# Performance work log

Measured on AMD Instinct MI355X. Metric: run time of the kernel, lower is better.

The kernel has to match this reference:

```python
import jax, jax.numpy as jnp
import numpy as np

N_NODES = 1_000_000
N_EDGES = 16_000_000
NUM_GRAPHS = 64
LATENT = 128
LAMBDA_LAP = 0.1
LAMBDA_DRIFT = 0.01
LAMBDA_ARAP = 0.1
BETA_WARMUP = 10
BETA_FINAL = 1.0


def setup_inputs() -> dict:
    key = jax.random.key(0)
    k1, k2, k3, k4, k5, k6 = jax.random.split(key, 6)
    return {
        "pred_output": jax.random.normal(k1, (N_NODES, 2), dtype=jnp.float32),
        "target": jax.random.normal(k2, (N_NODES, 2), dtype=jnp.float32),
        "edge_index": jax.random.randint(k3, (2, N_EDGES), 0, N_NODES, dtype=jnp.int32),
        "batch_indices": jnp.sort(jax.random.randint(k4, (N_NODES,), 0, NUM_GRAPHS, dtype=jnp.int32)),
        "mu": jax.random.normal(k5, (NUM_GRAPHS, LATENT), dtype=jnp.float32),
        "logvar": jax.random.normal(k6, (NUM_GRAPHS, LATENT), dtype=jnp.float32),
        "epoch": 5,
    }


def reference(pred_output, target, edge_index, batch_indices, mu, logvar, epoch):
    # reconstruction: MSE, mean over all elements
    recon = jnp.mean((pred_output - target) ** 2)

    # edge gather once; laplacian and ARAP reuse the same diff tensor
    i, j = edge_index[0], edge_index[1]
    diff = pred_output[i] - pred_output[j]                 # [E, 2]
    lap = jnp.sum(diff ** 2) / edge_index.shape[1]

    # drift suppression: per-graph mean displacement via segment_sum
    ones = jnp.ones((pred_output.shape[0],), dtype=pred_output.dtype)
    sums = jax.ops.segment_sum(pred_output, batch_indices, num_segments=NUM_GRAPHS)
    counts = jax.ops.segment_sum(ones, batch_indices, num_segments=NUM_GRAPHS)
    means = sums / counts[:, None]                         # [G, 2]
    drift = jnp.sum(means ** 2) / NUM_GRAPHS

    # ARAP: unbiased variance of edge lengths (torch.var default ddof=1)
    edge_len = jnp.sqrt(jnp.sum(diff ** 2, axis=1))        # [E]
    arap = jnp.var(edge_len, ddof=1)

    # KL divergence, mean over graphs
    kl = jnp.mean(-0.5 * jnp.sum(1.0 + logvar - mu ** 2 - jnp.exp(logvar), axis=1))

    # beta warmup (epoch is a static python int)
    beta = (epoch / BETA_WARMUP) * BETA_FINAL if epoch < BETA_WARMUP else BETA_FINAL

    total = recon + LAMBDA_LAP * lap + LAMBDA_DRIFT * drift + LAMBDA_ARAP * arap + beta * kl
    return total
```

## Files before the change

### kernel.cpp

```cpp
#include <hip/hip_runtime.h>
#include <hip/hip_fp16.h>
#include <math.h>

#define N_NODES    1000000
#define N_EDGES    16000000
#define NUM_GRAPHS 64
#define LATENT     128

#define WS_DOUBLES 200
#define PACKED_OFFSET 2048

typedef int vint4 __attribute__((ext_vector_type(4)));

__global__ void init_ws(double* ws) {
    int t = blockIdx.x * blockDim.x + threadIdx.x;
    if (t < WS_DOUBLES) ws[t] = 0.0;
}

__global__ void node_kl_pass(const float2* __restrict__ pred,
                             const float2* __restrict__ targ,
                             const int*    __restrict__ batch,
                             const float*  __restrict__ mu,
                             const float*  __restrict__ logvar,
                             double* __restrict__ ws,
                             unsigned* __restrict__ packed) {
    __shared__ float sgx[NUM_GRAPHS];
    __shared__ float sgy[NUM_GRAPHS];
    __shared__ int   scnt[NUM_GRAPHS];
    __shared__ double smem[8];

    for (int g = threadIdx.x; g < NUM_GRAPHS; g += blockDim.x) {
        sgx[g] = 0.f; sgy[g] = 0.f; scnt[g] = 0;
    }
    __syncthreads();

    float recon = 0.f;
    const int idx = blockIdx.x * blockDim.x + threadIdx.x;
    const int stride = gridDim.x * blockDim.x;
    for (int n = idx; n < N_NODES; n += stride) {
        float2 p = pred[n];
        float2 t = targ[n];
        float dx = p.x - t.x, dy = p.y - t.y;
        recon += dx * dx + dy * dy;

        if (packed) {
            __half2 h = __floats2half2_rn(p.x, p.y);
            packed[n] = *reinterpret_cast<unsigned*>(&h);
        }

        int b = batch[n];
        unsigned long long act = __ballot(1);
        int b0 = __shfl(b, 0);
        bool fast = (act == ~0ull) && (__ballot(b == b0) == act);
        if (fast) {
            float sx = p.x, sy = p.y;
            #pragma unroll
            for (int off = 32; off > 0; off >>= 1) {
                sx += __shfl_xor(sx, off);
                sy += __shfl_xor(sy, off);
            }
            if ((threadIdx.x & 63) == 0) {
                atomicAdd(&sgx[b0], sx);
                atomicAdd(&sgy[b0], sy);
                atomicAdd(&scnt[b0], 64);
            }
        } else {
            atomicAdd(&sgx[b], p.x);
            atomicAdd(&sgy[b], p.y);
            atomicAdd(&scnt[b], 1);
        }
    }

    double r = (double)recon;
    #pragma unroll
    for (int off = 32; off > 0; off >>= 1) r += __shfl_down(r, off);
    const int lane = threadIdx.x & 63;
    const int wid  = threadIdx.x >> 6;
    if (lane == 0) smem[wid] = r;
    __syncthreads();
    if (threadIdx.x == 0) {
        double tot = 0.0;
        const int nw = blockDim.x >> 6;
        for (int w = 0; w < nw; ++w) tot += smem[w];
        atomicAdd(&ws[0], tot);
    }

    for (int g = threadIdx.x; g < NUM_GRAPHS; g += blockDim.x) {
        if (scnt[g] != 0) {
            atomicAdd(&ws[4 + g],   (double)sgx[g]);
            atomicAdd(&ws[68 + g],  (double)sgy[g]);
            atomicAdd(&ws[132 + g], (double)scnt[g]);
        }
    }

    if (blockIdx.x == 0) {
        double s = 0.0;
        for (int t = threadIdx.x; t < NUM_GRAPHS * LATENT; t += blockDim.x) {
            float m = mu[t], lv = logvar[t];
            s += (double)(1.0f + lv - m * m - expf(lv));
        }
        #pragma unroll
        for (int off = 32; off > 0; off >>= 1) s += __shfl_down(s, off);
        __syncthreads();
        if (lane == 0) smem[wid] = s;
        __syncthreads();
        if (threadIdx.x == 0) {
            double tot = 0.0;
            const int nw = blockDim.x >> 6;
            for (int w = 0; w < nw; ++w) tot += smem[w];
            atomicAdd(&ws[3], tot);
        }
    }
}

__device__ __forceinline__ void edge_flush(float s1, float s2, double* ws,
                                           double* smem1, double* smem2) {
    double r1 = (double)s1, r2 = (double)s2;
    #pragma unroll
    for (int off = 32; off > 0; off >>= 1) {
        r1 += __shfl_down(r1, off);
        r2 += __shfl_down(r2, off);
    }
    const int lane = threadIdx.x & 63;
    const int wid  = threadIdx.x >> 6;
    if (lane == 0) { smem1[wid] = r1; smem2[wid] = r2; }
    __syncthreads();
    if (threadIdx.x == 0) {
        double t1 = 0.0, t2 = 0.0;
        const int nw = blockDim.x >> 6;
        for (int w = 0; w < nw; ++w) { t1 += smem1[w]; t2 += smem2[w]; }
        atomicAdd(&ws[1], t1);
        atomicAdd(&ws[2], t2);
    }
}

__device__ __forceinline__ vint4 ld_stream_x4(const vint4* p) {
    vint4 r;
    asm volatile("global_load_dwordx4 %0, %1, off sc0 sc1 nt"
                 : "=v"(r) : "v"(p) : "memory");
    return r;
}

__device__ __forceinline__ void acc_pair(unsigned pa, unsigned pb,
                                         float& s1, float& s2) {
    __half2 ha = *reinterpret_cast<__half2*>(&pa);
    __half2 hb = *reinterpret_cast<__half2*>(&pb);
    float2 fa = __half22float2(ha);
    float2 fb = __half22float2(hb);
    float dx = fa.x - fb.x, dy = fa.y - fb.y;
    float l2 = dx * dx + dy * dy;
    s2 += l2;
    s1 += sqrtf(l2);
}

__global__ void edge_pass_packed(const unsigned* __restrict__ packed,
                                 const int* __restrict__ ei,
                                 double* __restrict__ ws) {
    __shared__ double smem1[8];
    __shared__ double smem2[8];

    float s1 = 0.f, s2 = 0.f;
    const int gid = blockIdx.x * blockDim.x + threadIdx.x;
    const int stride = gridDim.x * blockDim.x;
    const int ngroups = N_EDGES / 8;
    const vint4* eia = (const vint4*)ei;
    const vint4* eib = (const vint4*)(ei + N_EDGES);

    int g = gid;
    if (g < ngroups) {
        vint4 a0 = ld_stream_x4(eia + 2 * g);
        vint4 a1 = ld_stream_x4(eia + 2 * g + 1);
        vint4 b0 = ld_stream_x4(eib + 2 * g);
        vint4 b1 = ld_stream_x4(eib + 2 * g + 1);
        asm volatile("s_waitcnt vmcnt(0)"
                     : "+v"(a0), "+v"(a1), "+v"(b0), "+v"(b1) :: "memory");
        __builtin_amdgcn_sched_barrier(0);
        while (true) {
            const int gn = g + stride;
            const bool more = gn < ngroups;
            vint4 a0n = {0,0,0,0}, a1n = {0,0,0,0};
            vint4 b0n = {0,0,0,0}, b1n = {0,0,0,0};
            if (more) {
                a0n = ld_stream_x4(eia + 2 * gn);
                a1n = ld_stream_x4(eia + 2 * gn + 1);
                b0n = ld_stream_x4(eib + 2 * gn);
                b1n = ld_stream_x4(eib + 2 * gn + 1);
            }

            unsigned qa0 = packed[a0.x], qb0 = packed[b0.x];
            unsigned qa1 = packed[a0.y], qb1 = packed[b0.y];
            unsigned qa2 = packed[a0.z], qb2 = packed[b0.z];
            unsigned qa3 = packed[a0.w], qb3 = packed[b0.w];
            unsigned qa4 = packed[a1.x], qb4 = packed[b1.x];
            unsigned qa5 = packed[a1.y], qb5 = packed[b1.y];
            unsigned qa6 = packed[a1.z], qb6 = packed[b1.z];
            unsigned qa7 = packed[a1.w], qb7 = packed[b1.w];

            acc_pair(qa0, qb0, s1, s2);
            acc_pair(qa1, qb1, s1, s2);
            acc_pair(qa2, qb2, s1, s2);
            acc_pair(qa3, qb3, s1, s2);
            acc_pair(qa4, qb4, s1, s2);
            acc_pair(qa5, qb5, s1, s2);
            acc_pair(qa6, qb6, s1, s2);
            acc_pair(qa7, qb7, s1, s2);

            if (!more) break;
            asm volatile("s_waitcnt vmcnt(0)"
                         : "+v"(a0n), "+v"(a1n), "+v"(b0n), "+v"(b1n) :: "memory");
            __builtin_amdgcn_sched_barrier(0);
            g = gn; a0 = a0n; a1 = a1n; b0 = b0n; b1 = b1n;
        }
    }
    asm volatile("s_waitcnt vmcnt(0)" ::: "memory");
    edge_flush(s1, s2, ws, smem1, smem2);
}

__global__ void edge_pass_f32(const float2* __restrict__ pred,
                              const int* __restrict__ ei,
                              double* __restrict__ ws) {
    __shared__ double smem1[8];
    __shared__ double smem2[8];

    float s1 = 0.f, s2 = 0.f;
    const int idx = blockIdx.x * blockDim.x + threadIdx.x;
    const int stride = gridDim.x * blockDim.x;
    for (int e = idx; e < N_EDGES; e += stride) {
        int i = ei[e];
        int j = ei[N_EDGES + e];
        float2 pi = pred[i];
        float2 pj = pred[j];
        float dx = pi.x - pj.x, dy = pi.y - pj.y;
        float l2 = dx * dx + dy * dy;
        s2 += l2;
        s1 += sqrtf(l2);
    }
    edge_flush(s1, s2, ws, smem1, smem2);
}

__global__ void finalize(const double* __restrict__ ws,
                         const int* __restrict__ epoch_p,
                         float* __restrict__ out) {
    double recon = ws[0] / (2.0 * (double)N_NODES);
    double S1 = ws[1], S2 = ws[2];
    double lap  = S2 / (double)N_EDGES;
    double arap = (S2 - S1 * S1 / (double)N_EDGES) / ((double)N_EDGES - 1.0);
    double drift = 0.0;
    for (int g = 0; g < NUM_GRAPHS; ++g) {
        double c  = ws[132 + g];
        double mx = ws[4 + g] / c;
        double my = ws[68 + g] / c;
        drift += mx * mx + my * my;
    }
    drift /= (double)NUM_GRAPHS;
    double kl = -0.5 * ws[3] / (double)NUM_GRAPHS;
    int epoch = *epoch_p;
    double beta = (epoch < 10) ? ((double)epoch / 10.0) : 1.0;
    out[0] = (float)(recon + 0.1 * lap + 0.01 * drift + 0.1 * arap + beta * kl);
}

extern "C" void kernel_launch(void* const* d_in, const int* in_sizes, int n_in,
                              void* d_out, int out_size, void* d_ws, size_t ws_size,
                              hipStream_t stream) {
    const float2* pred   = (const float2*)d_in[0];
    const float2* targ   = (const float2*)d_in[1];
    const int*    ei     = (const int*)d_in[2];
    const int*    batch  = (const int*)d_in[3];
    const float*  mu     = (const float*)d_in[4];
    const float*  logvar = (const float*)d_in[5];
    const int*    epoch  = (const int*)d_in[6];
    float* out = (float*)d_out;
    double* ws = (double*)d_ws;

    const bool use_packed = ws_size >= (size_t)PACKED_OFFSET + 4ull * N_NODES;
    unsigned* packed = use_packed
        ? (unsigned*)((char*)d_ws + PACKED_OFFSET) : (unsigned*)nullptr;

    init_ws<<<1, 256, 0, stream>>>(ws);
    node_kl_pass<<<1024, 256, 0, stream>>>(pred, targ, batch, mu, logvar, ws, packed);
    if (use_packed)
        edge_pass_packed<<<2048, 256, 0, stream>>>(packed, ei, ws);
    else
        edge_pass_f32<<<2048, 256, 0, stream>>>(pred, ei, ws);
    finalize<<<1, 1, 0, stream>>>(ws, epoch, out);
}
```

Measured before the change: 379.8 us.

## Split edge pass into four variant kernels, reorder gathers before prefetch, shard atomics

The edge pass now runs as four kernels over quarters of the edge list. Two use 8-edge groups and two use 16-edge groups, and each comes with and without the sc0 cache hint on the gathers. Inside the loop the node gathers are issued before the next index prefetch, with a partial vmcnt wait, so the gathers overlap the streaming index loads. Global double atomics are spread across shadow copies (8 for node stats, 16 for edge sums) and summed in finalize to reduce contention. The extra launches and the exploratory mix of variants add overhead and make the cause of any change unclear.

```diff
diff --git a/kernel.cpp b/kernel.cpp
--- a/kernel.cpp
+++ b/kernel.cpp
@@ -7,14 +7,21 @@
 #define NUM_GRAPHS 64
 #define LATENT     128
 
-#define WS_DOUBLES 200
-#define PACKED_OFFSET 2048
+#define SH_BASE        8
+#define SH_STRIDE      200
+#define NSHADOW_BIG    8
+#define EDGE_SH_BASE   1608
+#define EDGE_NSHADOW   16
+#define WS_DOUBLES_TOT 1736
+#define WS_DOUBLES_LEGACY 208
+#define PACKED_OFFSET_BIG    16384
+#define PACKED_OFFSET_LEGACY 2048
 
 typedef int vint4 __attribute__((ext_vector_type(4)));
 
-__global__ void init_ws(double* ws) {
+__global__ void init_ws(double* ws, int n) {
     int t = blockIdx.x * blockDim.x + threadIdx.x;
-    if (t < WS_DOUBLES) ws[t] = 0.0;
+    if (t < n) ws[t] = 0.0;
 }
 
 __global__ void node_kl_pass(const float2* __restrict__ pred,
@@ -23,7 +30,8 @@
                              const float*  __restrict__ mu,
                              const float*  __restrict__ logvar,
                              double* __restrict__ ws,
-                             unsigned* __restrict__ packed) {
+                             unsigned* __restrict__ packed,
+                             int ns) {
     __shared__ float sgx[NUM_GRAPHS];
     __shared__ float sgy[NUM_GRAPHS];
     __shared__ int   scnt[NUM_GRAPHS];
@@ -33,6 +41,8 @@
         sgx[g] = 0.f; sgy[g] = 0.f; scnt[g] = 0;
     }
     __syncthreads();
+
+    double* shbase = ws + SH_BASE + (size_t)(blockIdx.x & (ns - 1)) * SH_STRIDE;
 
     float recon = 0.f;
     const int idx = blockIdx.x * blockDim.x + threadIdx.x;
@@ -82,14 +92,14 @@
         double tot = 0.0;
         const int nw = blockDim.x >> 6;
         for (int w = 0; w < nw; ++w) tot += smem[w];
-        atomicAdd(&ws[0], tot);
+        atomicAdd(&shbase[0], tot);
     }
 
     for (int g = threadIdx.x; g < NUM_GRAPHS; g += blockDim.x) {
         if (scnt[g] != 0) {
-            atomicAdd(&ws[4 + g],   (double)sgx[g]);
-            atomicAdd(&ws[68 + g],  (double)sgy[g]);
-            atomicAdd(&ws[132 + g], (double)scnt[g]);
+            atomicAdd(&shbase[2 + g],   (double)sgx[g]);
+            atomicAdd(&shbase[66 + g],  (double)sgy[g]);
+            atomicAdd(&shbase[130 + g], (double)scnt[g]);
         }
     }
 
@@ -108,12 +118,13 @@
             double tot = 0.0;
             const int nw = blockDim.x >> 6;
             for (int w = 0; w < nw; ++w) tot += smem[w];
-            atomicAdd(&ws[3], tot);
+            atomicAdd(&shbase[1], tot);
         }
     }
 }
 
 __device__ __forceinline__ void edge_flush(float s1, float s2, double* ws,
+                                           int edge_mode,
                                            double* smem1, double* smem2) {
     double r1 = (double)s1, r2 = (double)s2;
     #pragma unroll
@@ -129,8 +140,14 @@
         double t1 = 0.0, t2 = 0.0;
         const int nw = blockDim.x >> 6;
         for (int w = 0; w < nw; ++w) { t1 += smem1[w]; t2 += smem2[w]; }
-        atomicAdd(&ws[1], t1);
-        atomicAdd(&ws[2], t2);
+        if (edge_mode) {
+            const int sh = blockIdx.x & (EDGE_NSHADOW - 1);
+            atomicAdd(&ws[EDGE_SH_BASE + sh * 8 + 0], t1);
+            atomicAdd(&ws[EDGE_SH_BASE + sh * 8 + 1], t2);
+        } else {
+            atomicAdd(&ws[1], t1);
+            atomicAdd(&ws[2], t2);
+        }
     }
 }
 
@@ -138,6 +155,18 @@
     vint4 r;
     asm volatile("global_load_dwordx4 %0, %1, off sc0 sc1 nt"
                  : "=v"(r) : "v"(p) : "memory");
+    return r;
+}
+
+template<bool SC0>
+__device__ __forceinline__ unsigned gth(const unsigned* base, int idx) {
+    unsigned r;
+    if constexpr (SC0)
+        asm volatile("global_load_dword %0, %1, %2 sc0"
+                     : "=v"(r) : "v"(idx * 4), "s"(base) : "memory");
+    else
+        asm volatile("global_load_dword %0, %1, %2"
+                     : "=v"(r) : "v"(idx * 4), "s"(base) : "memory");
     return r;
 }
 
@@ -153,72 +182,182 @@
     s1 += sqrtf(l2);
 }
 
-__global__ void edge_pass_packed(const unsigned* __restrict__ packed,
-                                 const int* __restrict__ ei,
-                                 double* __restrict__ ws) {
+template<bool SC0>
+__global__ void edge_pass8(const unsigned* __restrict__ packed,
+                           const int* __restrict__ ei,
+                           double* __restrict__ ws,
+                           int edge_mode, int g0, int ngroups) {
     __shared__ double smem1[8];
     __shared__ double smem2[8];
 
     float s1 = 0.f, s2 = 0.f;
     const int gid = blockIdx.x * blockDim.x + threadIdx.x;
     const int stride = gridDim.x * blockDim.x;
-    const int ngroups = N_EDGES / 8;
     const vint4* eia = (const vint4*)ei;
     const vint4* eib = (const vint4*)(ei + N_EDGES);
 
     int g = gid;
     if (g < ngroups) {
-        vint4 a0 = ld_stream_x4(eia + 2 * g);
-        vint4 a1 = ld_stream_x4(eia + 2 * g + 1);
-        vint4 b0 = ld_stream_x4(eib + 2 * g);
-        vint4 b1 = ld_stream_x4(eib + 2 * g + 1);
+        vint4 a0 = ld_stream_x4(eia + 2 * (g0 + g));
+        vint4 a1 = ld_stream_x4(eia + 2 * (g0 + g) + 1);
+        vint4 b0 = ld_stream_x4(eib + 2 * (g0 + g));
+        vint4 b1 = ld_stream_x4(eib + 2 * (g0 + g) + 1);
         asm volatile("s_waitcnt vmcnt(0)"
                      : "+v"(a0), "+v"(a1), "+v"(b0), "+v"(b1) :: "memory");
         __builtin_amdgcn_sched_barrier(0);
         while (true) {
+            unsigned q0  = gth<SC0>(packed, a0.x), q1  = gth<SC0>(packed, b0.x);
+            unsigned q2  = gth<SC0>(packed, a0.y), q3  = gth<SC0>(packed, b0.y);
+            unsigned q4  = gth<SC0>(packed, a0.z), q5  = gth<SC0>(packed, b0.z);
+            unsigned q6  = gth<SC0>(packed, a0.w), q7  = gth<SC0>(packed, b0.w);
+            unsigned q8  = gth<SC0>(packed, a1.x), q9  = gth<SC0>(packed, b1.x);
+            unsigned q10 = gth<SC0>(packed, a1.y), q11 = gth<SC0>(packed, b1.y);
+            unsigned q12 = gth<SC0>(packed, a1.z), q13 = gth<SC0>(packed, b1.z);
+            unsigned q14 = gth<SC0>(packed, a1.w), q15 = gth<SC0>(packed, b1.w);
+
             const int gn = g + stride;
             const bool more = gn < ngroups;
-            vint4 a0n = {0,0,0,0}, a1n = {0,0,0,0};
-            vint4 b0n = {0,0,0,0}, b1n = {0,0,0,0};
-            if (more) {
-                a0n = ld_stream_x4(eia + 2 * gn);
-                a1n = ld_stream_x4(eia + 2 * gn + 1);
-                b0n = ld_stream_x4(eib + 2 * gn);
-                b1n = ld_stream_x4(eib + 2 * gn + 1);
-            }
-
-            unsigned qa0 = packed[a0.x], qb0 = packed[b0.x];
-            unsigned qa1 = packed[a0.y], qb1 = packed[b0.y];
-            unsigned qa2 = packed[a0.z], qb2 = packed[b0.z];
-            unsigned qa3 = packed[a0.w], qb3 = packed[b0.w];
-            unsigned qa4 = packed[a1.x], qb4 = packed[b1.x];
-            unsigned qa5 = packed[a1.y], qb5 = packed[b1.y];
-            unsigned qa6 = packed[a1.z], qb6 = packed[b1.z];
-            unsigned qa7 = packed[a1.w], qb7 = packed[b1.w];
-
-            acc_pair(qa0, qb0, s1, s2);
-            acc_pair(qa1, qb1, s1, s2);
-            acc_pair(qa2, qb2, s1, s2);
-            acc_pair(qa3, qb3, s1, s2);
-            acc_pair(qa4, qb4, s1, s2);
-            acc_pair(qa5, qb5, s1, s2);
-            acc_pair(qa6, qb6, s1, s2);
-            acc_pair(qa7, qb7, s1, s2);
+            const int gs = g0 + (more ? gn : g);
+            vint4 A0 = ld_stream_x4(eia + 2 * gs);
+            vint4 A1 = ld_stream_x4(eia + 2 * gs + 1);
+            vint4 B0 = ld_stream_x4(eib + 2 * gs);
+            vint4 B1 = ld_stream_x4(eib + 2 * gs + 1);
+
+            asm volatile("s_waitcnt vmcnt(4)"
+                         : "+v"(q0), "+v"(q1), "+v"(q2), "+v"(q3),
+                           "+v"(q4), "+v"(q5), "+v"(q6), "+v"(q7),
+                           "+v"(q8), "+v"(q9), "+v"(q10), "+v"(q11),
+                           "+v"(q12), "+v"(q13), "+v"(q14), "+v"(q15)
+                         :: "memory");
+            __builtin_amdgcn_sched_barrier(0);
+
+            acc_pair(q0, q1, s1, s2);
+            acc_pair(q2, q3, s1, s2);
+            acc_pair(q4, q5, s1, s2);
+            acc_pair(q6, q7, s1, s2);
+            acc_pair(q8, q9, s1, s2);
+            acc_pair(q10, q11, s1, s2);
+            acc_pair(q12, q13, s1, s2);
+            acc_pair(q14, q15, s1, s2);
 
             if (!more) break;
             asm volatile("s_waitcnt vmcnt(0)"
-                         : "+v"(a0n), "+v"(a1n), "+v"(b0n), "+v"(b1n) :: "memory");
+                         : "+v"(A0), "+v"(A1), "+v"(B0), "+v"(B1) :: "memory");
             __builtin_amdgcn_sched_barrier(0);
-            g = gn; a0 = a0n; a1 = a1n; b0 = b0n; b1 = b1n;
+            g = gn; a0 = A0; a1 = A1; b0 = B0; b1 = B1;
         }
     }
     asm volatile("s_waitcnt vmcnt(0)" ::: "memory");
-    edge_flush(s1, s2, ws, smem1, smem2);
+    edge_flush(s1, s2, ws, edge_mode, smem1, smem2);
+}
+
+template<bool SC0>
+__global__ void edge_pass16(const unsigned* __restrict__ packed,
+                            const int* __restrict__ ei,
+                            double* __restrict__ ws,
+                            int edge_mode, int g0, int ngroups) {
+    __shared__ double smem1[8];
+    __shared__ double smem2[8];
+
+    float s1 = 0.f, s2 = 0.f;
+    const int gid = blockIdx.x * blockDim.x + threadIdx.x;
+    const int stride = gridDim.x * blockDim.x;
+    const vint4* eia = (const vint4*)ei;
+    const vint4* eib = (const vint4*)(ei + N_EDGES);
+
+    int g = gid;
+    if (g < ngroups) {
+        vint4 a0 = ld_stream_x4(eia + 4 * (g0 + g));
+        vint4 a1 = ld_stream_x4(eia + 4 * (g0 + g) + 1);
+        vint4 a2 = ld_stream_x4(eia + 4 * (g0 + g) + 2);
+        vint4 a3 = ld_stream_x4(eia + 4 * (g0 + g) + 3);
+        vint4 b0 = ld_stream_x4(eib + 4 * (g0 + g));
+        vint4 b1 = ld_stream_x4(eib + 4 * (g0 + g) + 1);
+        vint4 b2 = ld_stream_x4(eib + 4 * (g0 + g) + 2);
+        vint4 b3 = ld_stream_x4(eib + 4 * (g0 + g) + 3);
+        asm volatile("s_waitcnt vmcnt(0)"
+                     : "+v"(a0), "+v"(a1), "+v"(a2), "+v"(a3),
+                       "+v"(b0), "+v"(b1), "+v"(b2), "+v"(b3) :: "memory");
+        __builtin_amdgcn_sched_barrier(0);
+        while (true) {
+            unsigned q0  = gth<SC0>(packed, a0.x), q1  = gth<SC0>(packed, b0.x);
+            unsigned q2  = gth<SC0>(packed, a0.y), q3  = gth<SC0>(packed, b0.y);
+            unsigned q4  = gth<SC0>(packed, a0.z), q5  = gth<SC0>(packed, b0.z);
+            unsigned q6  = gth<SC0>(packed, a0.w), q7  = gth<SC0>(packed, b0.w);
+            unsigned q8  = gth<SC0>(packed, a1.x), q9  = gth<SC0>(packed, b1.x);
+            unsigned q10 = gth<SC0>(packed, a1.y), q11 = gth<SC0>(packed, b1.y);
+            unsigned q12 = gth<SC0>(packed, a1.z), q13 = gth<SC0>(packed, b1.z);
+            unsigned q14 = gth<SC0>(packed, a1.w), q15 = gth<SC0>(packed, b1.w);
+            unsigned q16 = gth<SC0>(packed, a2.x), q17 = gth<SC0>(packed, b2.x);
+            unsigned q18 = gth<SC0>(packed, a2.y), q19 = gth<SC0>(packed, b2.y);
+            unsigned q20 = gth<SC0>(packed, a2.z), q21 = gth<SC0>(packed, b2.z);
+            unsigned q22 = gth<SC0>(packed, a2.w), q23 = gth<SC0>(packed, b2.w);
+            unsigned q24 = gth<SC0>(packed, a3.x), q25 = gth<SC0>(packed, b3.x);
+            unsigned q26 = gth<SC0>(packed, a3.y), q27 = gth<SC0>(packed, b3.y);
+            unsigned q28 = gth<SC0>(packed, a3.z), q29 = gth<SC0>(packed, b3.z);
+            unsigned q30 = gth<SC0>(packed, a3.w), q31 = gth<SC0>(packed, b3.w);
+
+            const int gn = g + stride;
+            const bool more = gn < ngroups;
+            const int gs = g0 + (more ? gn : g);
+            vint4 A0 = ld_stream_x4(eia + 4 * gs);
+            vint4 A1 = ld_stream_x4(eia + 4 * gs + 1);
+            vint4 A2 = ld_stream_x4(eia + 4 * gs + 2);
+            vint4 A3 = ld_stream_x4(eia + 4 * gs + 3);
+            vint4 B0 = ld_stream_x4(eib + 4 * gs);
+            vint4 B1 = ld_stream_x4(eib + 4 * gs + 1);
+            vint4 B2 = ld_stream_x4(eib + 4 * gs + 2);
+            vint4 B3 = ld_stream_x4(eib + 4 * gs + 3);
+
+            asm volatile("s_waitcnt vmcnt(8)"
+                         : "+v"(q0), "+v"(q1), "+v"(q2), "+v"(q3),
+                           "+v"(q4), "+v"(q5), "+v"(q6), "+v"(q7),
+                           "+v"(q8), "+v"(q9), "+v"(q10), "+v"(q11),
+                           "+v"(q12), "+v"(q13), "+v"(q14), "+v"(q15)
+                         :: "memory");
+            asm volatile("s_waitcnt vmcnt(8)"
+                         : "+v"(q16), "+v"(q17), "+v"(q18), "+v"(q19),
+                           "+v"(q20), "+v"(q21), "+v"(q22), "+v"(q23),
+                           "+v"(q24), "+v"(q25), "+v"(q26), "+v"(q27),
+                           "+v"(q28), "+v"(q29), "+v"(q30), "+v"(q31)
+                         :: "memory");
+            __builtin_amdgcn_sched_barrier(0);
+
+            acc_pair(q0, q1, s1, s2);
+            acc_pair(q2, q3, s1, s2);
+            acc_pair(q4, q5, s1, s2);
+            acc_pair(q6, q7, s1, s2);
+            acc_pair(q8, q9, s1, s2);
+            acc_pair(q10, q11, s1, s2);
+            acc_pair(q12, q13, s1, s2);
+            acc_pair(q14, q15, s1, s2);
+            acc_pair(q16, q17, s1, s2);
+            acc_pair(q18, q19, s1, s2);
+            acc_pair(q20, q21, s1, s2);
+            acc_pair(q22, q23, s1, s2);
+            acc_pair(q24, q25, s1, s2);
+            acc_pair(q26, q27, s1, s2);
+            acc_pair(q28, q29, s1, s2);
+            acc_pair(q30, q31, s1, s2);
+
+            if (!more) break;
+            asm volatile("s_waitcnt vmcnt(0)"
+                         : "+v"(A0), "+v"(A1), "+v"(A2), "+v"(A3),
+                           "+v"(B0), "+v"(B1), "+v"(B2), "+v"(B3) :: "memory");
+            __builtin_amdgcn_sched_barrier(0);
+            g = gn;
+            a0 = A0; a1 = A1; a2 = A2; a3 = A3;
+            b0 = B0; b1 = B1; b2 = B2; b3 = B3;
+        }
+    }
+    asm volatile("s_waitcnt vmcnt(0)" ::: "memory");
+    edge_flush(s1, s2, ws, edge_mode, smem1, smem2);
 }
 
 __global__ void edge_pass_f32(const float2* __restrict__ pred,
                               const int* __restrict__ ei,
-                              double* __restrict__ ws) {
+                              double* __restrict__ ws,
+                              int edge_mode) {
     __shared__ double smem1[8];
     __shared__ double smem2[8];
 
@@ -235,25 +374,44 @@
         s2 += l2;
         s1 += sqrtf(l2);
     }
-    edge_flush(s1, s2, ws, smem1, smem2);
+    edge_flush(s1, s2, ws, edge_mode, smem1, smem2);
 }
 
 __global__ void finalize(const double* __restrict__ ws,
                          const int* __restrict__ epoch_p,
-                         float* __restrict__ out) {
-    double recon = ws[0] / (2.0 * (double)N_NODES);
-    double S1 = ws[1], S2 = ws[2];
+                         float* __restrict__ out,
+                         int ns, int edge_mode) {
+    double recon_sum = 0.0, kl_sum = 0.0;
+    for (int s = 0; s < ns; ++s) {
+        recon_sum += ws[SH_BASE + s * SH_STRIDE + 0];
+        kl_sum    += ws[SH_BASE + s * SH_STRIDE + 1];
+    }
+    double S1, S2;
+    if (edge_mode) {
+        S1 = 0.0; S2 = 0.0;
+        for (int s = 0; s < EDGE_NSHADOW; ++s) {
+            S1 += ws[EDGE_SH_BASE + s * 8 + 0];
+            S2 += ws[EDGE_SH_BASE + s * 8 + 1];
+        }
+    } else {
+        S1 = ws[1]; S2 = ws[2];
+    }
+    double recon = recon_sum / (2.0 * (double)N_NODES);
     double lap  = S2 / (double)N_EDGES;
     double arap = (S2 - S1 * S1 / (double)N_EDGES) / ((double)N_EDGES - 1.0);
     double drift = 0.0;
     for (int g = 0; g < NUM_GRAPHS; ++g) {
-        double c  = ws[132 + g];
-        double mx = ws[4 + g] / c;
-        double my = ws[68 + g] / c;
+        double c = 0.0, sx = 0.0, sy = 0.0;
+        for (int s = 0; s < ns; ++s) {
+            c  += ws[SH_BASE + s * SH_STRIDE + 130 + g];
+            sx += ws[SH_BASE + s * SH_STRIDE + 2 + g];
+            sy += ws[SH_BASE + s * SH_STRIDE + 66 + g];
+        }
+        double mx = sx / c, my = sy / c;
         drift += mx * mx + my * my;
     }
     drift /= (double)NUM_GRAPHS;
-    double kl = -0.5 * ws[3] / (double)NUM_GRAPHS;
+    double kl = -0.5 * kl_sum / (double)NUM_GRAPHS;
     int epoch = *epoch_p;
     double beta = (epoch < 10) ? ((double)epoch / 10.0) : 1.0;
     out[0] = (float)(recon + 0.1 * lap + 0.01 * drift + 0.1 * arap + beta * kl);
@@ -272,15 +430,37 @@
     float* out = (float*)d_out;
     double* ws = (double*)d_ws;
 
-    const bool use_packed = ws_size >= (size_t)PACKED_OFFSET + 4ull * N_NODES;
-    unsigned* packed = use_packed
-        ? (unsigned*)((char*)d_ws + PACKED_OFFSET) : (unsigned*)nullptr;
-
-    init_ws<<<1, 256, 0, stream>>>(ws);
-    node_kl_pass<<<1024, 256, 0, stream>>>(pred, targ, batch, mu, logvar, ws, packed);
-    if (use_packed)
-        edge_pass_packed<<<2048, 256, 0, stream>>>(packed, ei, ws);
-    else
-        edge_pass_f32<<<2048, 256, 0, stream>>>(pred, ei, ws);
-    finalize<<<1, 1, 0, stream>>>(ws, epoch, out);
-}
+    const size_t packed_bytes = 4ull * N_NODES;
+    int ns, edge_mode;
+    unsigned* packed;
+    if (ws_size >= (size_t)PACKED_OFFSET_BIG + packed_bytes) {
+        ns = NSHADOW_BIG; edge_mode = 1;
+        packed = (unsigned*)((char*)d_ws + PACKED_OFFSET_BIG);
+    } else if (ws_size >= (size_t)PACKED_OFFSET_LEGACY + packed_bytes) {
+        ns = 1; edge_mode = 0;
+        packed = (unsigned*)((char*)d_ws + PACKED_OFFSET_LEGACY);
+    } else {
+        ns = 1; edge_mode = 0;
+        packed = nullptr;
+    }
+    const int nz = edge_mode ? WS_DOUBLES_TOT : WS_DOUBLES_LEGACY;
+
+    init_ws<<<(nz + 255) / 256, 256, 0, stream>>>(ws, nz);
+    node_kl_pass<<<1024, 256, 0, stream>>>(pred, targ, batch, mu, logvar, ws,
+                                           packed, ns);
+    if (packed) {
+        const int q8  = N_EDGES / 8 / 4;
+        const int q16 = N_EDGES / 16 / 4;
+        edge_pass8<false><<<1024, 256, 0, stream>>>(packed, ei, ws, edge_mode,
+                                                    0, q8);
+        edge_pass8<true><<<1024, 256, 0, stream>>>(packed, ei, ws, edge_mode,
+                                                   q8, q8);
+        edge_pass16<false><<<1024, 256, 0, stream>>>(packed, ei, ws, edge_mode,
+                                                     2 * q16, q16);
+        edge_pass16<true><<<1024, 256, 0, stream>>>(packed, ei, ws, edge_mode,
+                                                    3 * q16, q16);
+    } else {
+        edge_pass_f32<<<2048, 256, 0, stream>>>(pred, ei, ws, edge_mode);
+    }
+    finalize<<<1, 1, 0, stream>>>(ws, epoch, out, ns, edge_mode);
+}
```

Result: slower. 451.7 us (+19.0%).
